# Optimization experiments

Measured on AMD Instinct MI355X. Metric: run time of the kernel, lower is better.

The kernel has to match this reference:

```python
import jax, jax.numpy as jnp
import numpy as np

WS = 7       # window_size
SHIFT = 3    # shift
NH = 4       # n_heads


def _rel_index(ws: int) -> np.ndarray:
    # matches torch.cartesian_prod(arange(ws), arange(ws)) ordering (second index fastest)
    coords = np.stack(np.meshgrid(np.arange(ws), np.arange(ws), indexing='ij'), -1).reshape(-1, 2)
    d = coords[:, None, :] - coords[None, :, :]
    idx = (d[..., 0] + ws - 1) * (2 * ws - 1) + d[..., 1] + ws - 1
    return idx.reshape(-1).astype(np.int32)  # [ws*ws*ws*ws]


def _ln(x, g, b, eps=1e-5):
    m = x.mean(-1, keepdims=True)
    v = ((x - m) ** 2).mean(-1, keepdims=True)
    return (x - m) / jnp.sqrt(v + eps) * g + b


def setup_inputs() -> dict:
    key = jax.random.key(0)
    ks = jax.random.split(key, 14)
    B, H, W, C = 64, 56, 56, 128
    hidden = int(C * 4.0)
    s = 0.02
    return {
        'x': jax.random.normal(ks[0], (B, H, W, C), jnp.float32),
        'norm1_g': jnp.ones((C,), jnp.float32),
        'norm1_b': jnp.zeros((C,), jnp.float32),
        'qkv_w': jax.random.normal(ks[1], (3 * C, C), jnp.float32) * s,
        'qkv_b': jnp.zeros((3 * C,), jnp.float32),
        'out_w': jax.random.normal(ks[2], (C, C), jnp.float32) * s,
        'out_b': jnp.zeros((C,), jnp.float32),
        'pe_table': jax.random.normal(ks[3], (NH, (2 * WS - 1) ** 2), jnp.float32) * s,
        'norm2_g': jnp.ones((C,), jnp.float32),
        'norm2_b': jnp.zeros((C,), jnp.float32),
        'mlp_w1': jax.random.normal(ks[4], (hidden, C), jnp.float32) * s,
        'mlp_b1': jnp.zeros((hidden,), jnp.float32),
        'mlp_w2': jax.random.normal(ks[5], (C, hidden), jnp.float32) * s,
        'mlp_b2': jnp.zeros((C,), jnp.float32),
    }


def reference(x, norm1_g, norm1_b, qkv_w, qkv_b, out_w, out_b, pe_table,
              norm2_g, norm2_b, mlp_w1, mlp_b1, mlp_w2, mlp_b2):
    B, H, W, C = x.shape
    nH, nW = H // WS, W // WS
    L = WS * WS
    hd = C // NH

    h = _ln(x, norm1_g, norm1_b)
    h = jnp.roll(h, (SHIFT, SHIFT), (1, 2))  # shifted windows (no inverse roll in source)

    # window partition: [B,H,W,C] -> [B*nH*nW, L, C]
    h = h.reshape(B, nH, WS, nW, WS, C).transpose(0, 1, 3, 2, 4, 5).reshape(B * nH * nW, L, C)

    qkv = h @ qkv_w.T + qkv_b  # [N, L, 3C]
    q, k, v = jnp.split(qkv, 3, axis=-1)
    to_heads = lambda t: t.reshape(-1, L, NH, hd).transpose(0, 2, 1, 3)  # [N,h,L,hd]
    q, k, v = to_heads(q), to_heads(k), to_heads(v)

    idx = jnp.asarray(_rel_index(WS))
    bias = pe_table[:, idx].reshape(NH, L, L)  # gathered relative position bias

    scores = jnp.einsum('nhqd,nhkd->nhqk', q, k) / jnp.sqrt(jnp.float32(hd)) + bias[None]
    attn = jax.nn.softmax(scores, axis=-1)
    o = jnp.einsum('nhqk,nhkd->nhqd', attn, v).transpose(0, 2, 1, 3).reshape(-1, L, C)
    o = o @ out_w.T + out_b

    # window unpartition: [B*nH*nW, L, C] -> [B,H,W,C]
    o = o.reshape(B, nH, nW, WS, WS, C).transpose(0, 1, 3, 2, 4, 5).reshape(B, H, W, C)

    h2 = _ln(o, norm2_g, norm2_b)
    y = jax.nn.gelu(h2 @ mlp_w1.T + mlp_b1, approximate=False) @ mlp_w2.T + mlp_b2
    return y
```

## Files before the change

### kernel.cpp

```cpp
#include <hip/hip_runtime.h>
#include <hip/hip_bf16.h>


#define NWIN 4096
#define HB 7440
#define KOFF 2568
#define VOFF 5136

typedef __attribute__((ext_vector_type(8))) short s8v;
typedef __attribute__((ext_vector_type(4))) float f4v;

__device__ __forceinline__ void split2(float v, unsigned short& h, unsigned short& l) {
    unsigned int b = __float_as_uint(v);
    h = (unsigned short)(b >> 16);
    float hf = __uint_as_float(b & 0xFFFF0000u);
    __hip_bfloat16 lo = __float2bfloat16(v - hf);
    l = *reinterpret_cast<unsigned short*>(&lo);
}
__device__ __forceinline__ unsigned short bfr(float v) {
    __hip_bfloat16 h = __float2bfloat16(v);
    return *reinterpret_cast<unsigned short*>(&h);
}

__global__ __launch_bounds__(256) void presplit_kernel(
    const float* __restrict__ qkvw, const float* __restrict__ outw,
    const float* __restrict__ w1, const float* __restrict__ w2,
    unsigned short* __restrict__ P)
{
    int i = blockIdx.x * 256 + threadIdx.x;
    if (i >= 196608) return;
    if (i < 49152) {
        float v = qkvw[i];
        if (i < 16384) v *= 0.17677669529663687f;
        unsigned short h, l; split2(v, h, l);
        P[i] = h; P[49152 + i] = l;
    } else if (i < 65536) {
        int j = i - 49152; float v = outw[j];
        unsigned short h, l; split2(v, h, l);
        P[98304 + j] = h; P[114688 + j] = l;
    } else if (i < 131072) {
        int j = i - 65536;
        P[131072 + j] = bfr(w1[j]);
    } else {
        int j = i - 131072;
        P[196608 + j] = bfr(w2[j]);
    }
}

__global__ __launch_bounds__(256) void ln_kernel(
    const float* __restrict__ inF,
    const float* __restrict__ g, const float* __restrict__ bta,
    unsigned short* __restrict__ outH, unsigned short* __restrict__ outL,
    int tbase)
{
    int tid = threadIdx.x;
    int wave = tid >> 6, lane = tid & 63;
    int local = blockIdx.x * 4 + wave;
    int t = tbase + local;
    int n = t / 49, l = t - n * 49;
    int b = n >> 6, wh = (n >> 3) & 7, ww = n & 7;
    int i = l / 7, j = l - i * 7;
    int hh = wh * 7 + i, wimg = ww * 7 + j;
    int sh = (hh + 53) % 56, sw = (wimg + 53) % 56;
    const float* ip = inF + (size_t)((b * 56 + sh) * 56 + sw) * 128;
    float v0 = ip[lane], v1 = ip[lane + 64];
    float s = v0 + v1, sq = v0 * v0 + v1 * v1;
    #pragma unroll
    for (int off = 32; off > 0; off >>= 1) { s += __shfl_xor(s, off); sq += __shfl_xor(sq, off); }
    float mean = s * (1.0f / 128.0f);
    float var  = sq * (1.0f / 128.0f) - mean * mean;
    float rstd = rsqrtf(var + 1e-5f);
    float r0 = (v0 - mean) * rstd * g[lane]      + bta[lane];
    float r1 = (v1 - mean) * rstd * g[lane + 64] + bta[lane + 64];
    unsigned short h0, l0, h1, l1;
    split2(r0, h0, l0); split2(r1, h1, l1);
    size_t o = (size_t)local * 128;
    outH[o + lane] = h0; outH[o + lane + 64] = h1;
    outL[o + lane] = l0; outL[o + lane + 64] = l1;
}

__global__ __launch_bounds__(256) void qkv_gemm(
    const unsigned short* __restrict__ Agh, const unsigned short* __restrict__ Agl,
    const unsigned short* __restrict__ W,
    const float* __restrict__ bias,
    unsigned short* __restrict__ OutQK, unsigned short* __restrict__ OutV,
    int M)
{
    __shared__ __align__(16) unsigned short Ah[64 * 132];
    __shared__ __align__(16) unsigned short Al[64 * 132];
    int tid = threadIdx.x;
    int m0 = blockIdx.y * 64, n0 = blockIdx.x * 64;
    for (int c = tid; c < 1024; c += 256) {
        int row = c >> 4, c8 = (c & 15) * 8;
        int ar = m0 + row; if (ar >= M) ar = M - 1;
        *reinterpret_cast<s8v*>(&Ah[row * 132 + c8]) =
            *reinterpret_cast<const s8v*>(Agh + (size_t)ar * 128 + c8);
        *reinterpret_cast<s8v*>(&Al[row * 132 + c8]) =
            *reinterpret_cast<const s8v*>(Agl + (size_t)ar * 128 + c8);
    }
    __syncthreads();
    int wv = tid >> 6, ln = tid & 63;
    int wm = wv & 1, wn = wv >> 1;
    int fm = ln & 15, fq = ln >> 4;
    const unsigned short* Wh = W;
    const unsigned short* Wl = W + 49152;
    f4v acc[2][2] = {};
    #pragma unroll
    for (int kk = 0; kk < 4; ++kk) {
        s8v fah[2], fal[2], fbh[2], fbl[2];
        #pragma unroll
        for (int t = 0; t < 2; ++t) {
            int ao = (wm * 32 + t * 16 + fm) * 132 + kk * 32 + fq * 8;
            fah[t] = *reinterpret_cast<const s8v*>(&Ah[ao]);
            fal[t] = *reinterpret_cast<const s8v*>(&Al[ao]);
            size_t wo = (size_t)(n0 + wn * 32 + t * 16 + fm) * 128 + kk * 32 + fq * 8;
            fbh[t] = *reinterpret_cast<const s8v*>(Wh + wo);
            fbl[t] = *reinterpret_cast<const s8v*>(Wl + wo);
        }
        #pragma unroll
        for (int tm = 0; tm < 2; ++tm)
            #pragma unroll
            for (int tn = 0; tn < 2; ++tn) {
                acc[tm][tn] = __builtin_amdgcn_mfma_f32_16x16x32_bf16(fah[tm], fbh[tn], acc[tm][tn], 0, 0, 0);
                acc[tm][tn] = __builtin_amdgcn_mfma_f32_16x16x32_bf16(fah[tm], fbl[tn], acc[tm][tn], 0, 0, 0);
                acc[tm][tn] = __builtin_amdgcn_mfma_f32_16x16x32_bf16(fal[tm], fbh[tn], acc[tm][tn], 0, 0, 0);
            }
    }
    #pragma unroll
    for (int tm = 0; tm < 2; ++tm)
        #pragma unroll
        for (int tn = 0; tn < 2; ++tn) {
            int col = n0 + wn * 32 + tn * 16 + fm;
            float bv = bias[col];
            if (col < 128) bv *= 0.17677669529663687f;
            #pragma unroll
            for (int r = 0; r < 4; ++r) {
                int m = m0 + wm * 32 + tm * 16 + fq * 4 + r;
                if (m >= M) continue;
                float v = acc[tm][tn][r] + bv;
                if (col < 256) {
                    OutQK[(size_t)m * 256 + col] = bfr(v);
                } else {
                    int dd = col - 256, hh = dd >> 5, d = dd & 31;
                    int win = m / 49, l2 = m - win * 49;
                    int kp = (l2 & 15) * 4 + (l2 >> 4);
                    OutV[((size_t)win * 128 + hh * 32 + d) * 64 + kp] = bfr(v);
                }
            }
        }
}

__global__ void bias_tab_kernel(const float* __restrict__ pe, float* __restrict__ tab) {
    int t = threadIdx.x;
    int h = t >> 6, ln = t & 63;
    int g = ln >> 4, c = ln & 15;
    for (int mt = 0; mt < 4; ++mt)
        for (int nt = 0; nt < 4; ++nt)
            for (int r = 0; r < 4; ++r) {
                int l1 = mt * 16 + g * 4 + r, l2 = nt * 16 + c;
                float b = 0.f;
                if (l1 < 49 && l2 < 49) {
                    int i1 = l1 / 7, j1 = l1 % 7, i2 = l2 / 7, j2 = l2 % 7;
                    b = pe[h * 169 + (i1 - i2 + 6) * 13 + (j1 - j2 + 6)];
                }
                tab[((h * 64 + ln) * 16 + mt * 4 + nt) * 4 + r] = b;
            }
}

__global__ __launch_bounds__(256) void attn_mfma(
    const unsigned short* __restrict__ qk,
    const unsigned short* __restrict__ vt,
    const float* __restrict__ btab,
    unsigned short* __restrict__ oH)
{
    __shared__ __align__(16) unsigned short lds[4 * HB];
    int tid = threadIdx.x;
    int win = blockIdx.x;
    const unsigned short* srcqk = qk + (size_t)win * 49 * 256;
    const unsigned short* srcv  = vt + (size_t)win * 8192;

    for (int idx = tid; idx < 1568; idx += 256) {
        int l2 = idx >> 5, c8 = idx & 31;
        int d8 = c8 * 8;
        s8v v8 = *reinterpret_cast<const s8v*>(srcqk + (size_t)l2 * 256 + d8);
        int sec = d8 >> 7, dd = d8 & 127, hh = dd >> 5, kk = dd & 31;
        *reinterpret_cast<s8v*>(&lds[hh * HB + (sec ? KOFF : 0) + l2 * 40 + kk]) = v8;
    }
    for (int idx = tid; idx < 1024; idx += 256) {
        int row = idx >> 3, j = idx & 7;
        s8v v8 = *reinterpret_cast<const s8v*>(srcv + (size_t)row * 64 + j * 8);
        int hh = row >> 5, d = row & 31;
        *reinterpret_cast<s8v*>(&lds[hh * HB + VOFF + d * 72 + j * 8]) = v8;
    }
    __syncthreads();
    for (int i = tid; i < 1920; i += 256) {
        int hh = i / 480, rem = i % 480, d = rem / 15, j = rem % 15;
        lds[hh * HB + VOFF + d * 72 + (j + 1) * 4 + 3] = 0;
    }
    __syncthreads();

    int h = tid >> 6, ln = tid & 63;
    int fm = ln & 15, fq = ln >> 4;
    int base = h * HB;

    s8v Qf[4], Kf[4];
    #pragma unroll
    for (int t = 0; t < 4; ++t) {
        Qf[t] = *reinterpret_cast<const s8v*>(&lds[base + (t * 16 + fm) * 40 + fq * 8]);
        Kf[t] = *reinterpret_cast<const s8v*>(&lds[base + KOFF + (t * 16 + fm) * 40 + fq * 8]);
    }
    f4v S[4][4] = {};
    #pragma unroll
    for (int mt = 0; mt < 4; ++mt)
        #pragma unroll
        for (int nt = 0; nt < 4; ++nt)
            S[mt][nt] = __builtin_amdgcn_mfma_f32_16x16x32_bf16(Qf[mt], Kf[nt], S[mt][nt], 0, 0, 0);
    #pragma unroll
    for (int mt = 0; mt < 4; ++mt)
        #pragma unroll
        for (int nt = 0; nt < 4; ++nt)
            S[mt][nt] += *reinterpret_cast<const f4v*>(&btab[((h * 64 + ln) * 16 + mt * 4 + nt) * 4]);

    float rcp[16];
    #pragma unroll
    for (int mt = 0; mt < 4; ++mt) {
        #pragma unroll
        for (int r = 0; r < 4; ++r) {
            float v0 = S[mt][0][r], v1 = S[mt][1][r], v2 = S[mt][2][r], v3 = S[mt][3][r];
            if (fm != 0) v3 = -1e30f;
            float mx = fmaxf(fmaxf(v0, v1), fmaxf(v2, v3));
            #pragma unroll
            for (int off = 1; off < 16; off <<= 1) mx = fmaxf(mx, __shfl_xor(mx, off));
            float e0 = __expf(v0 - mx), e1 = __expf(v1 - mx);
            float e2 = __expf(v2 - mx), e3 = __expf(v3 - mx);
            float sm = e0 + e1 + e2 + e3;
            #pragma unroll
            for (int off = 1; off < 16; off <<= 1) sm += __shfl_xor(sm, off);
            rcp[mt * 4 + r] = 1.0f / sm;
            int row = mt * 16 + fq * 4 + r;
            ushort4 pk = { bfr(e0), bfr(e1), bfr(e2), bfr(e3) };
            *reinterpret_cast<ushort4*>(&lds[base + row * 72 + fm * 4]) = pk;
        }
    }

    f4v O[4][2] = {};
    #pragma unroll
    for (int kt = 0; kt < 2; ++kt) {
        s8v Pf[4], Vf[2];
        #pragma unroll
        for (int mt = 0; mt < 4; ++mt)
            Pf[mt] = *reinterpret_cast<const s8v*>(&lds[base + (mt * 16 + fm) * 72 + kt * 32 + fq * 8]);
        #pragma unroll
        for (int nt = 0; nt < 2; ++nt)
            Vf[nt] = *reinterpret_cast<const s8v*>(&lds[base + VOFF + (nt * 16 + fm) * 72 + kt * 32 + fq * 8]);
        #pragma unroll
        for (int mt = 0; mt < 4; ++mt)
            #pragma unroll
            for (int nt = 0; nt < 2; ++nt)
                O[mt][nt] = __builtin_amdgcn_mfma_f32_16x16x32_bf16(Pf[mt], Vf[nt], O[mt][nt], 0, 0, 0);
    }

    size_t ob = (size_t)win * 49 * 128 + h * 32;
    #pragma unroll
    for (int mt = 0; mt < 4; ++mt)
        #pragma unroll
        for (int r = 0; r < 4; ++r) {
            int row = mt * 16 + fq * 4 + r;
            if (row < 49) {
                float sc = rcp[mt * 4 + r];
                #pragma unroll
                for (int nt = 0; nt < 2; ++nt)
                    oH[ob + (size_t)row * 128 + nt * 16 + fm] = bfr(O[mt][nt][r] * sc);
            }
        }
}

__global__ __launch_bounds__(256) void proj_ln(
    const unsigned short* __restrict__ Ag,
    const unsigned short* __restrict__ W,
    const float* __restrict__ bias,
    const float* __restrict__ g, const float* __restrict__ bta,
    unsigned short* __restrict__ Out, int M)
{
    __shared__ __align__(16) unsigned short As[64 * 132];
    __shared__ float red[2][2][64];
    int tid = threadIdx.x;
    int m0 = blockIdx.x * 64;
    for (int c = tid; c < 1024; c += 256) {
        int row = c >> 4, c8 = (c & 15) * 8;
        int ar = m0 + row; if (ar >= M) ar = M - 1;
        *reinterpret_cast<s8v*>(&As[row * 132 + c8]) =
            *reinterpret_cast<const s8v*>(Ag + (size_t)ar * 128 + c8);
    }
    __syncthreads();
    int wv = tid >> 6, ln = tid & 63;
    int wm = wv & 1, wn = wv >> 1;
    int fm = ln & 15, fq = ln >> 4;
    const unsigned short* Wh = W;
    const unsigned short* Wl = W + 16384;
    f4v acc[2][4] = {};
    #pragma unroll
    for (int kk = 0; kk < 4; ++kk) {
        s8v fa[2];
        #pragma unroll
        for (int t = 0; t < 2; ++t)
            fa[t] = *reinterpret_cast<const s8v*>(&As[(wm * 32 + t * 16 + fm) * 132 + kk * 32 + fq * 8]);
        #pragma unroll
        for (int tn = 0; tn < 4; ++tn) {
            size_t wo = (size_t)(wn * 64 + tn * 16 + fm) * 128 + kk * 32 + fq * 8;
            s8v bh = *reinterpret_cast<const s8v*>(Wh + wo);
            s8v bl = *reinterpret_cast<const s8v*>(Wl + wo);
            #pragma unroll
            for (int tm = 0; tm < 2; ++tm) {
                acc[tm][tn] = __builtin_amdgcn_mfma_f32_16x16x32_bf16(fa[tm], bh, acc[tm][tn], 0, 0, 0);
                acc[tm][tn] = __builtin_amdgcn_mfma_f32_16x16x32_bf16(fa[tm], bl, acc[tm][tn], 0, 0, 0);
            }
        }
    }
    float sumv[2][4], sqv[2][4];
    #pragma unroll
    for (int tm = 0; tm < 2; ++tm)
        #pragma unroll
        for (int r = 0; r < 4; ++r) {
            float s = 0.f, q = 0.f;
            #pragma unroll
            for (int tn = 0; tn < 4; ++tn) {
                float v = acc[tm][tn][r] + bias[wn * 64 + tn * 16 + fm];
                acc[tm][tn][r] = v;
                s += v; q += v * v;
            }
            #pragma unroll
            for (int off = 1; off < 16; off <<= 1) { s += __shfl_xor(s, off); q += __shfl_xor(q, off); }
            sumv[tm][r] = s; sqv[tm][r] = q;
        }
    if (fm == 0) {
        #pragma unroll
        for (int tm = 0; tm < 2; ++tm)
            #pragma unroll
            for (int r = 0; r < 4; ++r) {
                int row = wm * 32 + tm * 16 + fq * 4 + r;
                red[wn][0][row] = sumv[tm][r];
                red[wn][1][row] = sqv[tm][r];
            }
    }
    __syncthreads();
    #pragma unroll
    for (int tm = 0; tm < 2; ++tm)
        #pragma unroll
        for (int r = 0; r < 4; ++r) {
            int row = wm * 32 + tm * 16 + fq * 4 + r;
            int m = m0 + row;
            float s = red[0][0][row] + red[1][0][row];
            float q = red[0][1][row] + red[1][1][row];
            float mean = s * (1.0f / 128.0f);
            float var  = q * (1.0f / 128.0f) - mean * mean;
            float rstd = rsqrtf(var + 1e-5f);
            if (m < M) {
                #pragma unroll
                for (int tn = 0; tn < 4; ++tn) {
                    int n = wn * 64 + tn * 16 + fm;
                    float o = (acc[tm][tn][r] - mean) * rstd * g[n] + bta[n];
                    Out[(size_t)m * 128 + n] = bfr(o);
                }
            }
        }
}

__global__ __launch_bounds__(256) void gemm_w(
    const unsigned short* __restrict__ A, const unsigned short* __restrict__ W,
    const float* __restrict__ bias,
    float* __restrict__ OutF, unsigned short* __restrict__ OutH,
    int M, int N, int K, int mode, int tbase)
{
    __shared__ __align__(16) unsigned short As[64 * 40];
    __shared__ __align__(16) unsigned short Ws[128 * 40];
    int tid = threadIdx.x;
    int wv = tid >> 6, ln = tid & 63;
    int wm = wv & 1, wn = wv >> 1;
    int fm = ln & 15, fq = ln >> 4;
    int m0 = blockIdx.y * 64, n0 = blockIdx.x * 128;
    int sr = tid >> 2, sk = (tid & 3) * 8;
    int arow = m0 + sr; if (arow >= M) arow = M - 1;
    const unsigned short* pA  = A + (size_t)arow * K + sk;
    const unsigned short* pW0 = W + (size_t)(n0 + sr) * K + sk;
    const unsigned short* pW1 = W + (size_t)(n0 + 64 + sr) * K + sk;
    int so = sr * 40 + sk;

    f4v acc[2][4] = {};
    s8v ra, rw0, rw1;
    #define LOADK(k0) do { \
        ra  = *reinterpret_cast<const s8v*>(pA  + (k0)); \
        rw0 = *reinterpret_cast<const s8v*>(pW0 + (k0)); \
        rw1 = *reinterpret_cast<const s8v*>(pW1 + (k0)); } while (0)
    LOADK(0);
    for (int k0 = 0; k0 < K; k0 += 32) {
        *reinterpret_cast<s8v*>(&As[so]) = ra;
        *reinterpret_cast<s8v*>(&Ws[so]) = rw0;
        *reinterpret_cast<s8v*>(&Ws[2560 + so]) = rw1;
        __syncthreads();
        if (k0 + 32 < K) LOADK(k0 + 32);
        s8v fa[2], fb[4];
        #pragma unroll
        for (int t = 0; t < 2; ++t)
            fa[t] = *reinterpret_cast<const s8v*>(&As[(wm * 32 + t * 16 + fm) * 40 + fq * 8]);
        #pragma unroll
        for (int t = 0; t < 4; ++t)
            fb[t] = *reinterpret_cast<const s8v*>(&Ws[(wn * 64 + t * 16 + fm) * 40 + fq * 8]);
        #pragma unroll
        for (int tm = 0; tm < 2; ++tm)
            #pragma unroll
            for (int tn = 0; tn < 4; ++tn)
                acc[tm][tn] = __builtin_amdgcn_mfma_f32_16x16x32_bf16(fa[tm], fb[tn], acc[tm][tn], 0, 0, 0);
        __syncthreads();
    }
    #undef LOADK

    #pragma unroll
    for (int tm = 0; tm < 2; ++tm)
        #pragma unroll
        for (int tn = 0; tn < 4; ++tn) {
            int col = n0 + wn * 64 + tn * 16 + fm;
            float bv = bias[col];
            #pragma unroll
            for (int r = 0; r < 4; ++r) {
                int m = m0 + wm * 32 + tm * 16 + fq * 4 + r;
                if (m >= M) continue;
                float v = acc[tm][tn][r] + bv;
                if (mode == 1) {
                    v = 0.5f * v * (1.0f + erff(v * 0.70710678118654752f));
                    OutH[(size_t)m * N + col] = bfr(v);
                } else {
                    int t = tbase + m;
                    int n = t / 49, l = t - n * 49;
                    int b = n >> 6, wh_ = (n >> 3) & 7, ww = n & 7;
                    int i = l / 7, jj = l - i * 7;
                    size_t orow = (size_t)((b * 56 + wh_ * 7 + i) * 56 + ww * 7 + jj);
                    OutF[orow * N + col] = v;
                }
            }
        }
}

extern "C" void kernel_launch(void* const* d_in, const int* in_sizes, int n_in,
                              void* d_out, int out_size, void* d_ws, size_t ws_size,
                              hipStream_t stream) {
    const float* x    = (const float*)d_in[0];
    const float* n1g  = (const float*)d_in[1];
    const float* n1b  = (const float*)d_in[2];
    const float* qkvw = (const float*)d_in[3];
    const float* qkvb = (const float*)d_in[4];
    const float* outw = (const float*)d_in[5];
    const float* outb = (const float*)d_in[6];
    const float* pe   = (const float*)d_in[7];
    const float* n2g  = (const float*)d_in[8];
    const float* n2b  = (const float*)d_in[9];
    const float* w1   = (const float*)d_in[10];
    const float* b1   = (const float*)d_in[11];
    const float* w2   = (const float*)d_in[12];
    const float* b2   = (const float*)d_in[13];
    float* y = (float*)d_out;

    size_t wpc = NWIN;
    while (wpc > 8 && 589824 + wpc * 116736ULL > ws_size) wpc >>= 1;
    const int nchunks = (int)(NWIN / wpc);
    const size_t rows = wpc * 49;

    char* ws = (char*)d_ws;
    float* btab = (float*)ws;
    unsigned short* wpl = (unsigned short*)(ws + 65536);
    unsigned short* bufAh = (unsigned short*)(ws + 589824);
    unsigned short* bufAl = bufAh + rows * 128;
    unsigned short* bufQK = bufAl + rows * 128;
    unsigned short* bufV  = bufQK + rows * 256;
    unsigned short* bufH  = bufV + wpc * 8192;
    const int gy = (int)((rows + 63) / 64);

    presplit_kernel<<<768, 256, 0, stream>>>(qkvw, outw, w1, w2, wpl);
    bias_tab_kernel<<<1, 256, 0, stream>>>(pe, btab);

    for (int c = 0; c < nchunks; ++c) {
        int tbase = (int)(c * wpc * 49);
        ln_kernel<<<(int)(rows / 4), 256, 0, stream>>>(x, n1g, n1b, bufAh, bufAl, tbase);
        qkv_gemm<<<dim3(6, gy), 256, 0, stream>>>(bufAh, bufAl, wpl, qkvb, bufQK, bufV, (int)rows);
        attn_mfma<<<(int)wpc, 256, 0, stream>>>(bufQK, bufV, btab, bufAh);
        proj_ln<<<gy, 256, 0, stream>>>(bufAh, wpl + 98304, outb, n2g, n2b, bufAl, (int)rows);
        gemm_w<<<dim3(4, gy), 256, 0, stream>>>(
            bufAl, wpl + 131072, b1, nullptr, bufH, (int)rows, 512, 128, 1, 0);
        gemm_w<<<dim3(1, gy), 256, 0, stream>>>(
            bufH, wpl + 196608, b2, y, nullptr, (int)rows, 128, 512, 3, tbase);
    }
}
```

Before: 824.4 us.

## Fuse LayerNorm into QKV GEMM, stage weights in LDS, drop split-bf16 for out-proj

Removes the standalone LN kernel. The QKV GEMM now loads the shifted x rows directly, computes LayerNorm in registers and writes split hi/lo bf16 tiles into LDS one K-chunk at a time. This drops the write and read-back of the hi/lo activation buffers. The W tiles for the QKV GEMM and the projection GEMM are staged through LDS with register prefetch instead of being read from global per wave. The output projection weight is no longer split into hi/lo, which halves its MFMA count but lowers precision. The trade-off is that each of the 6 column blocks recomputes LN for its rows, and extra syncs are added per K-chunk.

```diff
diff --git a/kernel.cpp b/kernel.cpp
--- a/kernel.cpp
+++ b/kernel.cpp
@@ -35,87 +35,97 @@
         unsigned short h, l; split2(v, h, l);
         P[i] = h; P[49152 + i] = l;
     } else if (i < 65536) {
-        int j = i - 49152; float v = outw[j];
-        unsigned short h, l; split2(v, h, l);
-        P[98304 + j] = h; P[114688 + j] = l;
+        int j = i - 49152;
+        P[98304 + j] = bfr(outw[j]);
     } else if (i < 131072) {
         int j = i - 65536;
-        P[131072 + j] = bfr(w1[j]);
+        P[114688 + j] = bfr(w1[j]);
     } else {
         int j = i - 131072;
-        P[196608 + j] = bfr(w2[j]);
-    }
-}
-
-__global__ __launch_bounds__(256) void ln_kernel(
-    const float* __restrict__ inF,
+        P[180224 + j] = bfr(w2[j]);
+    }
+}
+
+__global__ __launch_bounds__(256) void ln_qkv(
+    const float* __restrict__ x,
     const float* __restrict__ g, const float* __restrict__ bta,
-    unsigned short* __restrict__ outH, unsigned short* __restrict__ outL,
-    int tbase)
-{
-    int tid = threadIdx.x;
-    int wave = tid >> 6, lane = tid & 63;
-    int local = blockIdx.x * 4 + wave;
-    int t = tbase + local;
-    int n = t / 49, l = t - n * 49;
-    int b = n >> 6, wh = (n >> 3) & 7, ww = n & 7;
-    int i = l / 7, j = l - i * 7;
-    int hh = wh * 7 + i, wimg = ww * 7 + j;
-    int sh = (hh + 53) % 56, sw = (wimg + 53) % 56;
-    const float* ip = inF + (size_t)((b * 56 + sh) * 56 + sw) * 128;
-    float v0 = ip[lane], v1 = ip[lane + 64];
-    float s = v0 + v1, sq = v0 * v0 + v1 * v1;
-    #pragma unroll
-    for (int off = 32; off > 0; off >>= 1) { s += __shfl_xor(s, off); sq += __shfl_xor(sq, off); }
-    float mean = s * (1.0f / 128.0f);
-    float var  = sq * (1.0f / 128.0f) - mean * mean;
-    float rstd = rsqrtf(var + 1e-5f);
-    float r0 = (v0 - mean) * rstd * g[lane]      + bta[lane];
-    float r1 = (v1 - mean) * rstd * g[lane + 64] + bta[lane + 64];
-    unsigned short h0, l0, h1, l1;
-    split2(r0, h0, l0); split2(r1, h1, l1);
-    size_t o = (size_t)local * 128;
-    outH[o + lane] = h0; outH[o + lane + 64] = h1;
-    outL[o + lane] = l0; outL[o + lane + 64] = l1;
-}
-
-__global__ __launch_bounds__(256) void qkv_gemm(
-    const unsigned short* __restrict__ Agh, const unsigned short* __restrict__ Agl,
     const unsigned short* __restrict__ W,
     const float* __restrict__ bias,
     unsigned short* __restrict__ OutQK, unsigned short* __restrict__ OutV,
-    int M)
+    int M, int tbase)
 {
-    __shared__ __align__(16) unsigned short Ah[64 * 132];
-    __shared__ __align__(16) unsigned short Al[64 * 132];
+    __shared__ __align__(16) unsigned short Ah[64 * 40];
+    __shared__ __align__(16) unsigned short Al[64 * 40];
+    __shared__ __align__(16) unsigned short Wh[64 * 40];
+    __shared__ __align__(16) unsigned short Wl[64 * 40];
     int tid = threadIdx.x;
     int m0 = blockIdx.y * 64, n0 = blockIdx.x * 64;
-    for (int c = tid; c < 1024; c += 256) {
-        int row = c >> 4, c8 = (c & 15) * 8;
-        int ar = m0 + row; if (ar >= M) ar = M - 1;
-        *reinterpret_cast<s8v*>(&Ah[row * 132 + c8]) =
-            *reinterpret_cast<const s8v*>(Agh + (size_t)ar * 128 + c8);
-        *reinterpret_cast<s8v*>(&Al[row * 132 + c8]) =
-            *reinterpret_cast<const s8v*>(Agl + (size_t)ar * 128 + c8);
-    }
-    __syncthreads();
+    int sr = tid >> 2, sq = (tid & 3) * 8;
+    int ar = m0 + sr; if (ar >= M) ar = M - 1;
+    int t = tbase + ar;
+    int n = t / 49, l = t - n * 49;
+    int b = n >> 6, wh_ = (n >> 3) & 7, ww = n & 7;
+    int i = l / 7, j = l - i * 7;
+    int sh = (wh_ * 7 + i + 53) % 56, sw = (ww * 7 + j + 53) % 56;
+    const float* ip = x + (size_t)((b * 56 + sh) * 56 + sw) * 128;
+
+    float v[4][8];
+    float s = 0.f, q2 = 0.f;
+    #pragma unroll
+    for (int kc = 0; kc < 4; ++kc) {
+        float4 a = *reinterpret_cast<const float4*>(ip + kc * 32 + sq);
+        float4 c = *reinterpret_cast<const float4*>(ip + kc * 32 + sq + 4);
+        v[kc][0] = a.x; v[kc][1] = a.y; v[kc][2] = a.z; v[kc][3] = a.w;
+        v[kc][4] = c.x; v[kc][5] = c.y; v[kc][6] = c.z; v[kc][7] = c.w;
+        #pragma unroll
+        for (int e = 0; e < 8; ++e) { s += v[kc][e]; q2 += v[kc][e] * v[kc][e]; }
+    }
+    s  += __shfl_xor(s, 1);  s  += __shfl_xor(s, 2);
+    q2 += __shfl_xor(q2, 1); q2 += __shfl_xor(q2, 2);
+    float mean = s * (1.0f / 128.0f);
+    float var  = q2 * (1.0f / 128.0f) - mean * mean;
+    float rstd = rsqrtf(var + 1e-5f);
+    unsigned short ah[4][8], al[4][8];
+    #pragma unroll
+    for (int kc = 0; kc < 4; ++kc)
+        #pragma unroll
+        for (int e = 0; e < 8; ++e) {
+            int c = kc * 32 + sq + e;
+            float r = (v[kc][e] - mean) * rstd * g[c] + bta[c];
+            split2(r, ah[kc][e], al[kc][e]);
+        }
+
     int wv = tid >> 6, ln = tid & 63;
     int wm = wv & 1, wn = wv >> 1;
     int fm = ln & 15, fq = ln >> 4;
-    const unsigned short* Wh = W;
-    const unsigned short* Wl = W + 49152;
+    const unsigned short* Whg = W;
+    const unsigned short* Wlg = W + 49152;
+    size_t wrow = (size_t)(n0 + sr) * 128 + sq;
+    int so = sr * 40 + sq;
+    s8v rwh = *reinterpret_cast<const s8v*>(Whg + wrow);
+    s8v rwl = *reinterpret_cast<const s8v*>(Wlg + wrow);
+
     f4v acc[2][2] = {};
     #pragma unroll
-    for (int kk = 0; kk < 4; ++kk) {
+    for (int kc = 0; kc < 4; ++kc) {
+        *reinterpret_cast<s8v*>(&Ah[so]) = *reinterpret_cast<const s8v*>(ah[kc]);
+        *reinterpret_cast<s8v*>(&Al[so]) = *reinterpret_cast<const s8v*>(al[kc]);
+        *reinterpret_cast<s8v*>(&Wh[so]) = rwh;
+        *reinterpret_cast<s8v*>(&Wl[so]) = rwl;
+        __syncthreads();
+        if (kc < 3) {
+            rwh = *reinterpret_cast<const s8v*>(Whg + wrow + (kc + 1) * 32);
+            rwl = *reinterpret_cast<const s8v*>(Wlg + wrow + (kc + 1) * 32);
+        }
         s8v fah[2], fal[2], fbh[2], fbl[2];
         #pragma unroll
-        for (int t = 0; t < 2; ++t) {
-            int ao = (wm * 32 + t * 16 + fm) * 132 + kk * 32 + fq * 8;
-            fah[t] = *reinterpret_cast<const s8v*>(&Ah[ao]);
-            fal[t] = *reinterpret_cast<const s8v*>(&Al[ao]);
-            size_t wo = (size_t)(n0 + wn * 32 + t * 16 + fm) * 128 + kk * 32 + fq * 8;
-            fbh[t] = *reinterpret_cast<const s8v*>(Wh + wo);
-            fbl[t] = *reinterpret_cast<const s8v*>(Wl + wo);
+        for (int tt = 0; tt < 2; ++tt) {
+            int ao = (wm * 32 + tt * 16 + fm) * 40 + fq * 8;
+            fah[tt] = *reinterpret_cast<const s8v*>(&Ah[ao]);
+            fal[tt] = *reinterpret_cast<const s8v*>(&Al[ao]);
+            int bo = (wn * 32 + tt * 16 + fm) * 40 + fq * 8;
+            fbh[tt] = *reinterpret_cast<const s8v*>(&Wh[bo]);
+            fbl[tt] = *reinterpret_cast<const s8v*>(&Wl[bo]);
         }
         #pragma unroll
         for (int tm = 0; tm < 2; ++tm)
@@ -125,7 +135,9 @@
                 acc[tm][tn] = __builtin_amdgcn_mfma_f32_16x16x32_bf16(fah[tm], fbl[tn], acc[tm][tn], 0, 0, 0);
                 acc[tm][tn] = __builtin_amdgcn_mfma_f32_16x16x32_bf16(fal[tm], fbh[tn], acc[tm][tn], 0, 0, 0);
             }
-    }
+        __syncthreads();
+    }
+
     #pragma unroll
     for (int tm = 0; tm < 2; ++tm)
         #pragma unroll
@@ -137,14 +149,14 @@
             for (int r = 0; r < 4; ++r) {
                 int m = m0 + wm * 32 + tm * 16 + fq * 4 + r;
                 if (m >= M) continue;
-                float v = acc[tm][tn][r] + bv;
+                float vv = acc[tm][tn][r] + bv;
                 if (col < 256) {
-                    OutQK[(size_t)m * 256 + col] = bfr(v);
+                    OutQK[(size_t)m * 256 + col] = bfr(vv);
                 } else {
                     int dd = col - 256, hh = dd >> 5, d = dd & 31;
                     int win = m / 49, l2 = m - win * 49;
                     int kp = (l2 & 15) * 4 + (l2 >> 4);
-                    OutV[((size_t)win * 128 + hh * 32 + d) * 64 + kp] = bfr(v);
+                    OutV[((size_t)win * 128 + hh * 32 + d) * 64 + kp] = bfr(vv);
                 }
             }
         }
@@ -277,12 +289,13 @@
 
 __global__ __launch_bounds__(256) void proj_ln(
     const unsigned short* __restrict__ Ag,
-    const unsigned short* __restrict__ W,
+    const unsigned short* __restrict__ Wg,
     const float* __restrict__ bias,
     const float* __restrict__ g, const float* __restrict__ bta,
     unsigned short* __restrict__ Out, int M)
 {
     __shared__ __align__(16) unsigned short As[64 * 132];
+    __shared__ __align__(16) unsigned short Ws[128 * 40];
     __shared__ float red[2][2][64];
     int tid = threadIdx.x;
     int m0 = blockIdx.x * 64;
@@ -292,30 +305,36 @@
         *reinterpret_cast<s8v*>(&As[row * 132 + c8]) =
             *reinterpret_cast<const s8v*>(Ag + (size_t)ar * 128 + c8);
     }
-    __syncthreads();
+    int w0r = tid >> 2, w0c = (tid & 3) * 8;
+    int w1r = 64 + w0r;
+    s8v rw0 = *reinterpret_cast<const s8v*>(Wg + (size_t)w0r * 128 + w0c);
+    s8v rw1 = *reinterpret_cast<const s8v*>(Wg + (size_t)w1r * 128 + w0c);
+
     int wv = tid >> 6, ln = tid & 63;
     int wm = wv & 1, wn = wv >> 1;
     int fm = ln & 15, fq = ln >> 4;
-    const unsigned short* Wh = W;
-    const unsigned short* Wl = W + 16384;
     f4v acc[2][4] = {};
-    #pragma unroll
-    for (int kk = 0; kk < 4; ++kk) {
-        s8v fa[2];
+    for (int kc = 0; kc < 4; ++kc) {
+        *reinterpret_cast<s8v*>(&Ws[w0r * 40 + w0c]) = rw0;
+        *reinterpret_cast<s8v*>(&Ws[w1r * 40 + w0c]) = rw1;
+        __syncthreads();
+        if (kc < 3) {
+            rw0 = *reinterpret_cast<const s8v*>(Wg + (size_t)w0r * 128 + (kc + 1) * 32 + w0c);
+            rw1 = *reinterpret_cast<const s8v*>(Wg + (size_t)w1r * 128 + (kc + 1) * 32 + w0c);
+        }
+        s8v fa[2], fb[4];
         #pragma unroll
         for (int t = 0; t < 2; ++t)
-            fa[t] = *reinterpret_cast<const s8v*>(&As[(wm * 32 + t * 16 + fm) * 132 + kk * 32 + fq * 8]);
-        #pragma unroll
-        for (int tn = 0; tn < 4; ++tn) {
-            size_t wo = (size_t)(wn * 64 + tn * 16 + fm) * 128 + kk * 32 + fq * 8;
-            s8v bh = *reinterpret_cast<const s8v*>(Wh + wo);
-            s8v bl = *reinterpret_cast<const s8v*>(Wl + wo);
-            #pragma unroll
-            for (int tm = 0; tm < 2; ++tm) {
-                acc[tm][tn] = __builtin_amdgcn_mfma_f32_16x16x32_bf16(fa[tm], bh, acc[tm][tn], 0, 0, 0);
-                acc[tm][tn] = __builtin_amdgcn_mfma_f32_16x16x32_bf16(fa[tm], bl, acc[tm][tn], 0, 0, 0);
-            }
-        }
+            fa[t] = *reinterpret_cast<const s8v*>(&As[(wm * 32 + t * 16 + fm) * 132 + kc * 32 + fq * 8]);
+        #pragma unroll
+        for (int t = 0; t < 4; ++t)
+            fb[t] = *reinterpret_cast<const s8v*>(&Ws[(wn * 64 + t * 16 + fm) * 40 + fq * 8]);
+        #pragma unroll
+        for (int tm = 0; tm < 2; ++tm)
+            #pragma unroll
+            for (int tn = 0; tn < 4; ++tn)
+                acc[tm][tn] = __builtin_amdgcn_mfma_f32_16x16x32_bf16(fa[tm], fb[tn], acc[tm][tn], 0, 0, 0);
+        __syncthreads();
     }
     float sumv[2][4], sqv[2][4];
     #pragma unroll
@@ -358,9 +377,9 @@
             if (m < M) {
                 #pragma unroll
                 for (int tn = 0; tn < 4; ++tn) {
-                    int n = wn * 64 + tn * 16 + fm;
-                    float o = (acc[tm][tn][r] - mean) * rstd * g[n] + bta[n];
-                    Out[(size_t)m * 128 + n] = bfr(o);
+                    int nn = wn * 64 + tn * 16 + fm;
+                    float o = (acc[tm][tn][r] - mean) * rstd * g[nn] + bta[nn];
+                    Out[(size_t)m * 128 + nn] = bfr(o);
                 }
             }
         }
@@ -461,18 +480,18 @@
     float* y = (float*)d_out;
 
     size_t wpc = NWIN;
-    while (wpc > 8 && 589824 + wpc * 116736ULL > ws_size) wpc >>= 1;
+    while (wpc > 8 && 557056 + wpc * 116736ULL > ws_size) wpc >>= 1;
     const int nchunks = (int)(NWIN / wpc);
     const size_t rows = wpc * 49;
 
     char* ws = (char*)d_ws;
     float* btab = (float*)ws;
     unsigned short* wpl = (unsigned short*)(ws + 65536);
-    unsigned short* bufAh = (unsigned short*)(ws + 589824);
-    unsigned short* bufAl = bufAh + rows * 128;
-    unsigned short* bufQK = bufAl + rows * 128;
+    unsigned short* bufQK = (unsigned short*)(ws + 557056);
     unsigned short* bufV  = bufQK + rows * 256;
-    unsigned short* bufH  = bufV + wpc * 8192;
+    unsigned short* bufO  = bufV + wpc * 8192;
+    unsigned short* bufL  = bufO + rows * 128;
+    unsigned short* bufH  = bufL + rows * 128;
     const int gy = (int)((rows + 63) / 64);
 
     presplit_kernel<<<768, 256, 0, stream>>>(qkvw, outw, w1, w2, wpl);
@@ -480,13 +499,13 @@
 
     for (int c = 0; c < nchunks; ++c) {
         int tbase = (int)(c * wpc * 49);
-        ln_kernel<<<(int)(rows / 4), 256, 0, stream>>>(x, n1g, n1b, bufAh, bufAl, tbase);
-        qkv_gemm<<<dim3(6, gy), 256, 0, stream>>>(bufAh, bufAl, wpl, qkvb, bufQK, bufV, (int)rows);
-        attn_mfma<<<(int)wpc, 256, 0, stream>>>(bufQK, bufV, btab, bufAh);
-        proj_ln<<<gy, 256, 0, stream>>>(bufAh, wpl + 98304, outb, n2g, n2b, bufAl, (int)rows);
+        ln_qkv<<<dim3(6, gy), 256, 0, stream>>>(
+            x, n1g, n1b, wpl, qkvb, bufQK, bufV, (int)rows, tbase);
+        attn_mfma<<<(int)wpc, 256, 0, stream>>>(bufQK, bufV, btab, bufO);
+        proj_ln<<<gy, 256, 0, stream>>>(bufO, wpl + 98304, outb, n2g, n2b, bufL, (int)rows);
         gemm_w<<<dim3(4, gy), 256, 0, stream>>>(
-            bufAl, wpl + 131072, b1, nullptr, bufH, (int)rows, 512, 128, 1, 0);
+            bufL, wpl + 114688, b1, nullptr, bufH, (int)rows, 512, 128, 1, 0);
         gemm_w<<<dim3(1, gy), 256, 0, stream>>>(
-            bufH, wpl + 196608, b2, y, nullptr, (int)rows, 128, 512, 3, tbase);
-    }
-}
+            bufH, wpl + 180224, b2, y, nullptr, (int)rows, 128, 512, 3, tbase);
+    }
+}
```

After: 709.3 us. 14.0% less time.
